# Performance work log

Hardware: AMD Instinct MI355X
Metric: run time of the kernel (lower is better)

Reference implementation:

```python
import jax, jax.numpy as jnp
import numpy as np

N_INST = 2_000_000   # total instances
D_IN = 32
D_HID = 64
D_OUT = 1
NUM_BAGS = 100_000   # ids in [0, NUM_BAGS)


def setup_inputs() -> dict:
    key = jax.random.key(0)
    k0, k1, k2, k3, k4 = jax.random.split(key, 5)
    x = jax.random.normal(k0, (N_INST, D_IN), dtype=jnp.float32)
    # sorted bag ids, every bag present (contiguous bags of equal size -> a
    # valid instance of sorted_randint over [0, NUM_BAGS))
    ids = (jnp.arange(N_INST, dtype=jnp.int32) // (N_INST // NUM_BAGS))[None, :]
    W1 = jax.random.normal(k1, (D_IN, D_HID), dtype=jnp.float32) / np.sqrt(D_IN)
    b1 = jax.random.normal(k2, (D_HID,), dtype=jnp.float32) * 0.01
    W2 = jax.random.normal(k3, (D_HID, D_OUT), dtype=jnp.float32) / np.sqrt(D_HID)
    b2 = jax.random.normal(k4, (D_OUT,), dtype=jnp.float32) * 0.01
    return {"x": x, "ids": ids, "W1": W1, "b1": b1, "W2": W2, "b2": b2}


def reference(x, ids, W1, b1, W2, b2):
    inner_ids = ids[-1]                                    # [N] bag id per instance
    h = jax.nn.relu(x @ W1 + b1)                           # prepNN: [N, D_HID]
    # fused segment mean over bags (replaces the Python loop + boolean masks)
    sums = jax.ops.segment_sum(h, inner_ids, num_segments=NUM_BAGS)          # [B, D_HID]
    counts = jax.ops.segment_sum(jnp.ones((h.shape[0],), h.dtype), inner_ids,
                                 num_segments=NUM_BAGS)                      # [B]
    pooled = sums / counts[:, None]                        # aggregation_func = mean
    out = pooled @ W2 + b2                                 # afterNN: [B, D_OUT]
    return out
```

## Files before the change

kernel.cpp:

```cpp
#include <hip/hip_runtime.h>

typedef __attribute__((ext_vector_type(8))) short short8v;
typedef __attribute__((ext_vector_type(4))) float f32x4;

__device__ __forceinline__ unsigned short f2bf(float f) {
  unsigned u = __builtin_bit_cast(unsigned, f);
  unsigned r = u + 0x7FFFu + ((u >> 16) & 1u);
  return (unsigned short)(r >> 16);
}
__device__ __forceinline__ float bf2f(unsigned short h) {
  unsigned u = ((unsigned)h) << 16;
  return __builtin_bit_cast(float, u);
}

__global__ void __launch_bounds__(256) bag_mlp_mfma(
    const float* __restrict__ x, const int* __restrict__ ids,
    const float* __restrict__ W1, const float* __restrict__ b1,
    const float* __restrict__ W2,
    float* __restrict__ bag_sum, int ntiles, int tiles_per_wave)
{
  const int lane = threadIdx.x & 63;
  const int lm = lane & 15;
  const int lg = lane >> 4;
  const int wave = blockIdx.x * (blockDim.x >> 6) + (threadIdx.x >> 6);

  const int t0 = wave * tiles_per_wave;
  const int t1 = min(t0 + tiles_per_wave, ntiles);
  if (t0 >= t1) return;

  short8v bh[4], bl[4];
#pragma unroll
  for (int nt = 0; nt < 4; ++nt) {
    const int col = lm + 16 * nt;
#pragma unroll
    for (int e = 0; e < 8; ++e) {
      const int k = 16 * (e >> 2) + 4 * lg + (e & 3);
      const float f = W1[k * 64 + col];
      const unsigned short h = f2bf(f);
      bh[nt][e] = (short)h;
      bl[nt][e] = (short)f2bf(f - bf2f(h));
    }
  }
  float b1c[4], w2c[4];
#pragma unroll
  for (int nt = 0; nt < 4; ++nt) {
    b1c[nt] = b1[lm + 16 * nt];
    w2c[nt] = W2[lm + 16 * nt];
  }

  float4 va, vb; int4 iv;
  {
    const long base = (long)t0 * 16;
    const float* p = x + (base + lm) * 32 + 4 * lg;
    va = *(const float4*)p;
    vb = *(const float4*)(p + 16);
    if (lm == 0) iv = *(const int4*)(ids + base + 4 * lg);
  }

  for (int t = t0; t < t1; ++t) {
    float4 nva, nvb; int4 niv;
    if (t + 1 < t1) {
      const long base = (long)(t + 1) * 16;
      const float* p = x + (base + lm) * 32 + 4 * lg;
      nva = *(const float4*)p;
      nvb = *(const float4*)(p + 16);
      if (lm == 0) niv = *(const int4*)(ids + base + 4 * lg);
    }

    short8v ah, al;
#pragma unroll
    for (int j = 0; j < 4; ++j) {
      const float f = ((const float*)&va)[j];
      const unsigned short h = f2bf(f);
      ah[j] = (short)h; al[j] = (short)f2bf(f - bf2f(h));
      const float g = ((const float*)&vb)[j];
      const unsigned short h2 = f2bf(g);
      ah[4 + j] = (short)h2; al[4 + j] = (short)f2bf(g - bf2f(h2));
    }

    f32x4 acc[4];
#pragma unroll
    for (int nt = 0; nt < 4; ++nt) {
      f32x4 a = {0.f, 0.f, 0.f, 0.f};
      a = __builtin_amdgcn_mfma_f32_16x16x32_bf16(ah, bh[nt], a, 0, 0, 0);
      a = __builtin_amdgcn_mfma_f32_16x16x32_bf16(ah, bl[nt], a, 0, 0, 0);
      a = __builtin_amdgcn_mfma_f32_16x16x32_bf16(al, bh[nt], a, 0, 0, 0);
      acc[nt] = a;
    }

    float ps[4];
#pragma unroll
    for (int r = 0; r < 4; ++r) {
      float s = 0.f;
#pragma unroll
      for (int nt = 0; nt < 4; ++nt) {
        const float h = acc[nt][r] + b1c[nt];
        s = fmaf(fmaxf(h, 0.f), w2c[nt], s);
      }
      ps[r] = s;
    }
#pragma unroll
    for (int m = 1; m < 16; m <<= 1) {
#pragma unroll
      for (int r = 0; r < 4; ++r) ps[r] += __shfl_xor(ps[r], m, 64);
    }

    if (lm == 0) {
      float a0 = ps[0], a1 = ps[1], a2 = ps[2], a3 = ps[3];
      const int i0 = iv.x, i1 = iv.y, i2 = iv.z, i3 = iv.w;
      if (i1 == i0) a1 += a0; else atomicAdd(&bag_sum[i0], a0);
      if (i2 == i1) a2 += a1; else atomicAdd(&bag_sum[i1], a1);
      if (i3 == i2) a3 += a2; else atomicAdd(&bag_sum[i2], a2);
      atomicAdd(&bag_sum[i3], a3);
    }

    va = nva; vb = nvb; iv = niv;
  }
}

__global__ void __launch_bounds__(256) finalize_kernel(
    const float* __restrict__ bag_sum, const int* __restrict__ ids,
    const float* __restrict__ b2, float* __restrict__ out, int nbags, int n)
{
  const int b = blockIdx.x * blockDim.x + threadIdx.x;
  if (b >= nbags) return;
  int lo0 = 0, hi0 = n;
  while (lo0 < hi0) { const int mid = (lo0 + hi0) >> 1; if (ids[mid] < b) lo0 = mid + 1; else hi0 = mid; }
  int lo1 = lo0, hi1 = n;
  while (lo1 < hi1) { const int mid = (lo1 + hi1) >> 1; if (ids[mid] < b + 1) lo1 = mid + 1; else hi1 = mid; }
  const float c = (float)(lo1 - lo0);
  out[b] = bag_sum[b] / c + b2[0];
}

extern "C" void kernel_launch(void* const* d_in, const int* in_sizes, int n_in,
                              void* d_out, int out_size, void* d_ws, size_t ws_size,
                              hipStream_t stream)
{
  const float* x   = (const float*)d_in[0];
  const int*   ids = (const int*)d_in[1];
  const float* W1  = (const float*)d_in[2];
  const float* b1  = (const float*)d_in[3];
  const float* W2  = (const float*)d_in[4];
  const float* b2  = (const float*)d_in[5];
  float* out = (float*)d_out;

  const int n     = in_sizes[0] / 32;
  const int nbags = out_size;

  float* bag_sum = (float*)d_ws;
  hipMemsetAsync(bag_sum, 0, (size_t)nbags * sizeof(float), stream);

  const int ntiles  = n / 16;
  const int nblocks = 2048;
  const int nwaves  = nblocks * 4;
  const int tpw     = (ntiles + nwaves - 1) / nwaves;

  bag_mlp_mfma<<<nblocks, 256, 0, stream>>>(x, ids, W1, b1, W2, bag_sum,
                                            ntiles, tpw);
  finalize_kernel<<<(nbags + 255) / 256, 256, 0, stream>>>(bag_sum, ids, b2,
                                                           out, nbags, n);
}
```

Measured before the change: 372.0 us.

## Stage x via async global-to-LDS loads, 64-row chunks, LDS bag accumulation

Rewrites the main kernel to process 64-row chunks per wave, staging x tiles into swizzled LDS with global_load_lds and double-issuing the next chunk while computing. Per-row results are reduced with DPP instead of shuffles and accumulated into a per-wave LDS slot array keyed by bag offset, with one global atomic per slot at the end. The finalize kernel's per-bag binary searches over ids are replaced by a separate kernel that records bag start indices. This aims to cut global atomics, shuffle overhead and the search cost, but adds an extra kernel launch and relies on sorted ids with bags fitting in 64 slots per wave.

```diff
diff --git a/kernel.cpp b/kernel.cpp
--- a/kernel.cpp
+++ b/kernel.cpp
@@ -1,7 +1,12 @@
 #include <hip/hip_runtime.h>
 
 typedef __attribute__((ext_vector_type(8))) short short8v;
+typedef __attribute__((ext_vector_type(4))) int   int4v;
 typedef __attribute__((ext_vector_type(4))) float f32x4;
+
+#define NBLOCKS 1024
+#define WPB 4
+#define NSLOT 64
 
 __device__ __forceinline__ unsigned short f2bf(float f) {
   unsigned u = __builtin_bit_cast(unsigned, f);
@@ -13,20 +18,32 @@
   return __builtin_bit_cast(float, u);
 }
 
-__global__ void __launch_bounds__(256) bag_mlp_mfma(
+template <int CTRL>
+__device__ __forceinline__ float dpp_add(float s) {
+  int t = __builtin_amdgcn_update_dpp(0, __builtin_bit_cast(int, s), CTRL, 0xF, 0xF, true);
+  return s + __builtin_bit_cast(float, t);
+}
+
+__global__ void __launch_bounds__(256) bag_mlp_v3(
     const float* __restrict__ x, const int* __restrict__ ids,
     const float* __restrict__ W1, const float* __restrict__ b1,
     const float* __restrict__ W2,
-    float* __restrict__ bag_sum, int ntiles, int tiles_per_wave)
-{
+    float* __restrict__ bag_sum, int nchunks, int cpw, int nbags)
+{
+  __shared__ __align__(16) char stage[WPB][8192];
+  __shared__ float sacc[WPB][NSLOT];
+
+  const int wid  = threadIdx.x >> 6;
   const int lane = threadIdx.x & 63;
-  const int lm = lane & 15;
-  const int lg = lane >> 4;
-  const int wave = blockIdx.x * (blockDim.x >> 6) + (threadIdx.x >> 6);
-
-  const int t0 = wave * tiles_per_wave;
-  const int t1 = min(t0 + tiles_per_wave, ntiles);
-  if (t0 >= t1) return;
+  const int lm = lane & 15, lg = lane >> 4;
+  const int w = blockIdx.x * WPB + wid;
+
+  const int c_begin = w * cpw;
+  if (c_begin >= nchunks) return;
+  const int c_end = min(c_begin + cpw, nchunks);
+
+  sacc[wid][lane] = 0.f;
+  const int base_id = ids[(size_t)c_begin * 64];
 
   short8v bh[4], bl[4];
 #pragma unroll
@@ -48,88 +65,124 @@
     w2c[nt] = W2[lm + 16 * nt];
   }
 
-  float4 va, vb; int4 iv;
-  {
-    const long base = (long)t0 * 16;
-    const float* p = x + (base + lm) * 32 + 4 * lg;
-    va = *(const float4*)p;
-    vb = *(const float4*)(p + 16);
-    if (lm == 0) iv = *(const int4*)(ids + base + 4 * lg);
-  }
-
-  for (int t = t0; t < t1; ++t) {
-    float4 nva, nvb; int4 niv;
-    if (t + 1 < t1) {
-      const long base = (long)(t + 1) * 16;
-      const float* p = x + (base + lm) * 32 + 4 * lg;
-      nva = *(const float4*)p;
-      nvb = *(const float4*)(p + 16);
-      if (lm == 0) niv = *(const int4*)(ids + base + 4 * lg);
-    }
-
-    short8v ah, al;
-#pragma unroll
-    for (int j = 0; j < 4; ++j) {
-      const float f = ((const float*)&va)[j];
-      const unsigned short h = f2bf(f);
-      ah[j] = (short)h; al[j] = (short)f2bf(f - bf2f(h));
-      const float g = ((const float*)&vb)[j];
-      const unsigned short h2 = f2bf(g);
-      ah[4 + j] = (short)h2; al[4 + j] = (short)f2bf(g - bf2f(h2));
-    }
-
-    f32x4 acc[4];
-#pragma unroll
-    for (int nt = 0; nt < 4; ++nt) {
-      f32x4 a = {0.f, 0.f, 0.f, 0.f};
-      a = __builtin_amdgcn_mfma_f32_16x16x32_bf16(ah, bh[nt], a, 0, 0, 0);
-      a = __builtin_amdgcn_mfma_f32_16x16x32_bf16(ah, bl[nt], a, 0, 0, 0);
-      a = __builtin_amdgcn_mfma_f32_16x16x32_bf16(al, bh[nt], a, 0, 0, 0);
-      acc[nt] = a;
-    }
-
-    float ps[4];
-#pragma unroll
-    for (int r = 0; r < 4; ++r) {
-      float s = 0.f;
+  const int R_perm = ((lm >> 2) << 4) + (lg << 2) + (lm & 3);
+
+  auto issue_stage = [&](int c) {
+    const float* src0 = x + (size_t)c * 2048;
+#pragma unroll
+    for (int q = 0; q < 8; ++q) {
+      const int g   = q * 64 + lane;
+      const int row = g >> 3;
+      const int sl  = (g & 7) ^ (row & 7);
+      const float* src = src0 + row * 32 + sl * 4;
+      __builtin_amdgcn_global_load_lds(
+          (const __attribute__((address_space(1))) void*)src,
+          (__attribute__((address_space(3))) void*)(&stage[wid][q * 1024]),
+          16, 0, 0);
+    }
+  };
+
+  issue_stage(c_begin);
+
+  for (int c = c_begin; c < c_end; ++c) {
+    asm volatile("s_waitcnt vmcnt(0)" ::: "memory");
+
+    const int myid = ids[(size_t)c * 64 + R_perm];
+
+    short8v ah[4], al[4];
+    const char* sb = &stage[wid][0];
+#pragma unroll
+    for (int t = 0; t < 4; ++t) {
+      const int rb = t * 2048 + lm * 128;
+      const float4 va = *(const float4*)(sb + rb + ((lg ^ (lm & 7)) << 4));
+      const float4 vb = *(const float4*)(sb + rb + (((lg + 4) ^ (lm & 7)) << 4));
+      int4v ahi, ali;
+#pragma unroll
+      for (int j = 0; j < 4; ++j) {
+        const float f0 = (j < 2) ? ((j == 0) ? va.x : va.z) : ((j == 2) ? vb.x : vb.z);
+        const float f1 = (j < 2) ? ((j == 0) ? va.y : va.w) : ((j == 2) ? vb.y : vb.w);
+        const unsigned u0 = __builtin_bit_cast(unsigned, f0);
+        const unsigned u1 = __builtin_bit_cast(unsigned, f1);
+        const unsigned r0 = u0 + 0x7FFFu + ((u0 >> 16) & 1u);
+        const unsigned r1 = u1 + 0x7FFFu + ((u1 >> 16) & 1u);
+        const unsigned h0 = r0 & 0xFFFF0000u, h1 = r1 & 0xFFFF0000u;
+        const float lo0 = f0 - __builtin_bit_cast(float, h0);
+        const float lo1 = f1 - __builtin_bit_cast(float, h1);
+        ahi[j] = (int)((r0 >> 16) | h1);
+        ali[j] = (int)(((unsigned)f2bf(lo0)) | (((unsigned)f2bf(lo1)) << 16));
+      }
+      ah[t] = __builtin_bit_cast(short8v, ahi);
+      al[t] = __builtin_bit_cast(short8v, ali);
+    }
+
+    asm volatile("s_waitcnt lgkmcnt(0)" ::: "memory");
+    const int cnext = (c + 1 < c_end) ? c + 1 : c;
+    issue_stage(cnext);
+
+    float myval = 0.f;
+#pragma unroll
+    for (int t = 0; t < 4; ++t) {
+      f32x4 acc[4];
+#pragma unroll
+      for (int nt = 0; nt < 4; ++nt)
+        acc[nt] = (f32x4){b1c[nt], b1c[nt], b1c[nt], b1c[nt]};
 #pragma unroll
       for (int nt = 0; nt < 4; ++nt) {
-        const float h = acc[nt][r] + b1c[nt];
-        s = fmaf(fmaxf(h, 0.f), w2c[nt], s);
-      }
-      ps[r] = s;
-    }
-#pragma unroll
-    for (int m = 1; m < 16; m <<= 1) {
-#pragma unroll
-      for (int r = 0; r < 4; ++r) ps[r] += __shfl_xor(ps[r], m, 64);
-    }
-
-    if (lm == 0) {
-      float a0 = ps[0], a1 = ps[1], a2 = ps[2], a3 = ps[3];
-      const int i0 = iv.x, i1 = iv.y, i2 = iv.z, i3 = iv.w;
-      if (i1 == i0) a1 += a0; else atomicAdd(&bag_sum[i0], a0);
-      if (i2 == i1) a2 += a1; else atomicAdd(&bag_sum[i1], a1);
-      if (i3 == i2) a3 += a2; else atomicAdd(&bag_sum[i2], a2);
-      atomicAdd(&bag_sum[i3], a3);
-    }
-
-    va = nva; vb = nvb; iv = niv;
+        acc[nt] = __builtin_amdgcn_mfma_f32_16x16x32_bf16(ah[t], bh[nt], acc[nt], 0, 0, 0);
+        acc[nt] = __builtin_amdgcn_mfma_f32_16x16x32_bf16(ah[t], bl[nt], acc[nt], 0, 0, 0);
+        acc[nt] = __builtin_amdgcn_mfma_f32_16x16x32_bf16(al[t], bh[nt], acc[nt], 0, 0, 0);
+      }
+      float ps[4];
+#pragma unroll
+      for (int r = 0; r < 4; ++r) {
+        float s = 0.f;
+#pragma unroll
+        for (int nt = 0; nt < 4; ++nt)
+          s = fmaf(fmaxf(acc[nt][r], 0.f), w2c[nt], s);
+        ps[r] = s;
+      }
+#pragma unroll
+      for (int r = 0; r < 4; ++r) {
+        ps[r] = dpp_add<0xB1>(ps[r]);
+        ps[r] = dpp_add<0x4E>(ps[r]);
+        ps[r] = dpp_add<0x124>(ps[r]);
+        ps[r] = dpp_add<0x128>(ps[r]);
+      }
+      const float t01 = (lm & 1) ? ps[1] : ps[0];
+      const float t23 = (lm & 1) ? ps[3] : ps[2];
+      const float sel = (lm & 2) ? t23 : t01;
+      if ((lm >> 2) == t) myval = sel;
+    }
+
+    const int slot = myid - base_id;
+    if (slot < NSLOT) atomicAdd(&sacc[wid][slot], myval);
+    else              atomicAdd(&bag_sum[myid], myval);
+  }
+
+  const float v = sacc[wid][lane];
+  const int bag = base_id + lane;
+  if (v != 0.f && bag < nbags) atomicAdd(&bag_sum[bag], v);
+}
+
+__global__ void __launch_bounds__(256) bag_start_kernel(
+    const int* __restrict__ ids, int* __restrict__ start, int n)
+{
+  for (int i = blockIdx.x * blockDim.x + threadIdx.x; i < n;
+       i += gridDim.x * blockDim.x) {
+    const int id = ids[i];
+    if (i == 0 || ids[i - 1] != id) start[id] = i;
   }
 }
 
 __global__ void __launch_bounds__(256) finalize_kernel(
-    const float* __restrict__ bag_sum, const int* __restrict__ ids,
+    const float* __restrict__ bag_sum, const int* __restrict__ start,
     const float* __restrict__ b2, float* __restrict__ out, int nbags, int n)
 {
   const int b = blockIdx.x * blockDim.x + threadIdx.x;
   if (b >= nbags) return;
-  int lo0 = 0, hi0 = n;
-  while (lo0 < hi0) { const int mid = (lo0 + hi0) >> 1; if (ids[mid] < b) lo0 = mid + 1; else hi0 = mid; }
-  int lo1 = lo0, hi1 = n;
-  while (lo1 < hi1) { const int mid = (lo1 + hi1) >> 1; if (ids[mid] < b + 1) lo1 = mid + 1; else hi1 = mid; }
-  const float c = (float)(lo1 - lo0);
-  out[b] = bag_sum[b] / c + b2[0];
+  const int s = start[b];
+  const int e = (b + 1 < nbags) ? start[b + 1] : n;
+  out[b] = bag_sum[b] / (float)(e - s) + b2[0];
 }
 
 extern "C" void kernel_launch(void* const* d_in, const int* in_sizes, int n_in,
@@ -148,15 +201,17 @@
   const int nbags = out_size;
 
   float* bag_sum = (float*)d_ws;
-  hipMemsetAsync(bag_sum, 0, (size_t)nbags * sizeof(float), stream);
-
-  const int ntiles  = n / 16;
-  const int nblocks = 2048;
-  const int nwaves  = nblocks * 4;
-  const int tpw     = (ntiles + nwaves - 1) / nwaves;
-
-  bag_mlp_mfma<<<nblocks, 256, 0, stream>>>(x, ids, W1, b1, W2, bag_sum,
-                                            ntiles, tpw);
-  finalize_kernel<<<(nbags + 255) / 256, 256, 0, stream>>>(bag_sum, ids, b2,
+  int*   start   = (int*)(bag_sum + nbags);
+
+  (void)hipMemsetAsync(bag_sum, 0, (size_t)nbags * sizeof(float), stream);
+
+  const int nchunks = n / 64;
+  const int nwaves  = NBLOCKS * WPB;
+  const int cpw     = (nchunks + nwaves - 1) / nwaves;
+
+  bag_mlp_v3<<<NBLOCKS, 256, 0, stream>>>(x, ids, W1, b1, W2, bag_sum,
+                                          nchunks, cpw, nbags);
+  bag_start_kernel<<<2048, 256, 0, stream>>>(ids, start, n);
+  finalize_kernel<<<(nbags + 255) / 256, 256, 0, stream>>>(bag_sum, start, b2,
                                                            out, nbags, n);
 }
```

Result: no change. 366.5 us (-1.5%).
